# Optimization experiments

Measured on AMD Instinct MI355X. Metric: run time of the kernel, lower is better.

## Reference

```python
import jax, jax.numpy as jnp
import numpy as np

B, L, H, N = 4, 4096, 1024, 64
LN_EPS = 1e-5


def setup_inputs() -> dict:
    key = jax.random.key(0)
    ks = jax.random.split(key, 6)
    x = jax.random.normal(ks[0], (B, L, H), dtype=jnp.float32)
    # S4D-Lin style init
    log_A_real = jnp.log(0.5 * jnp.ones((H, N), dtype=jnp.float32))
    A_imag = jnp.broadcast_to(jnp.pi * jnp.arange(N, dtype=jnp.float32), (H, N))
    C_re = jax.random.normal(ks[1], (H, N), dtype=jnp.float32) * 0.5
    C_im = jax.random.normal(ks[2], (H, N), dtype=jnp.float32) * 0.5
    # dt log-uniform in [1e-3, 1e-1]
    u = jax.random.uniform(ks[3], (H,), dtype=jnp.float32)
    log_dt = u * (jnp.log(0.1) - jnp.log(0.001)) + jnp.log(0.001)
    D = jax.random.normal(ks[4], (H,), dtype=jnp.float32)
    ln_w = jnp.ones((H,), dtype=jnp.float32)
    ln_b = jnp.zeros((H,), dtype=jnp.float32)
    return {"x": x, "log_A_real": log_A_real, "A_imag": A_imag,
            "C_re": C_re, "C_im": C_im, "log_dt": log_dt, "D": D,
            "ln_w": ln_w, "ln_b": ln_b}


def _s4d_kernel(log_A_real, A_imag, C_re, C_im, log_dt, length):
    # A: [H, N] complex with negative real part (stability)
    A = -jnp.exp(log_A_real) + 1j * A_imag
    dt = jnp.exp(log_dt)[:, None]                      # [H, 1]
    dtA = dt * A                                       # [H, N]
    C = C_re + 1j * C_im                               # [H, N]
    # ZOH discretization: Bbar*C -> C * (exp(dtA)-1)/A
    Ct = C * (jnp.exp(dtA) - 1.0) / A                  # [H, N]
    l = jnp.arange(length, dtype=jnp.float32)
    # Vandermonde: exp(dtA * l) over [H, N, L]
    V = jnp.exp(dtA[:, :, None] * l[None, None, :])
    K = 2.0 * jnp.real(jnp.einsum('hn,hnl->hl', Ct, V))  # [H, L]
    return K


def reference(x, log_A_real, A_imag, C_re, C_im, log_dt, D, ln_w, ln_b):
    b, length, h = x.shape
    K = _s4d_kernel(log_A_real, A_imag, C_re, C_im, log_dt, length)  # [H, L]
    # causal convolution via FFT, channels last: x is [B, L, H]
    n = 2 * length
    Xf = jnp.fft.rfft(x, n=n, axis=1)                  # [B, n//2+1, H]
    Kf = jnp.fft.rfft(K, n=n, axis=1)                  # [H, n//2+1]
    y = jnp.fft.irfft(Xf * Kf.T[None, :, :], n=n, axis=1)[:, :length, :]
    z = y + x * D[None, None, :]
    # dropout is identity in eval mode; residual + LayerNorm
    r = x + z
    mu = jnp.mean(r, axis=-1, keepdims=True)
    var = jnp.var(r, axis=-1, keepdims=True)
    out = (r - mu) * jax.lax.rsqrt(var + LN_EPS) * ln_w + ln_b
    return out
```

## Files before the change

kernel.cpp:

```cpp
#include <hip/hip_runtime.h>
#include <cstdint>

#define Bb 4
#define Lseq 4096
#define Hh 1024
#define Nst 64
constexpr float LN_EPS = 1e-5f;

typedef _Float16 f16x8 __attribute__((ext_vector_type(8)));
typedef _Float16 f16x4 __attribute__((ext_vector_type(4)));
typedef float f32x4v __attribute__((ext_vector_type(4)));

__global__ __launch_bounds__(256) void k_precompute(
    const float* __restrict__ logA, const float* __restrict__ Aim,
    const float* __restrict__ Cre, const float* __restrict__ Cim,
    const float* __restrict__ logdt, _Float16* __restrict__ mats,
    float* __restrict__ wwR, float* __restrict__ wwI) {
    __shared__ float sdAr[64], sdAi[64], scR[64], scI[64], sK[64];
    const int h = blockIdx.x, tid = threadIdx.x;
    _Float16* g = mats + (size_t)h * 20480;

    if (tid < 64) {
        const int n = tid, idx = h * 64 + n;
        const float ar = -expf(logA[idx]), ai = Aim[idx];
        const float dt = expf(logdt[h]);
        const float dAr = dt * ar, dAi = dt * ai;
        const float em = expf(dAr);
        const float wr = em * cosf(dAi), wi = em * sinf(dAi);
        const float Er = wr - 1.0f, Ei = wi;
        const float cr = Cre[idx], ci = Cim[idx];
        const float nr = cr * Er - ci * Ei, ni = cr * Ei + ci * Er;
        const float invd = 1.0f / (ar * ar + ai * ai);
        const float CtR = (nr * ar + ni * ai) * invd;
        const float CtI = (ni * ar - nr * ai) * invd;
        sdAr[n] = dAr; sdAi[n] = dAi; scR[n] = 2.0f * CtR; scI[n] = 2.0f * CtI;
        const float e64 = expf(dAr * 64.0f), a64 = dAi * 64.0f;
        wwR[idx] = e64 * cosf(a64);
        wwI[idx] = e64 * sinf(a64);
    }
    __syncthreads();

    for (int e = tid; e < 4096; e += 256) {
        const int row = e >> 6, colj = e & 63;
        {
            const float p = (float)(63 - colj);
            const float ee = expf(sdAr[row] * p), ang = sdAi[row] * p;
            g[e]        = (_Float16)(ee * cosf(ang));
            g[4096 + e] = (_Float16)(ee * sinf(ang));
        }
        {
            const int n = colj;
            const float q = (float)(row + 1);
            const float ee = expf(sdAr[n] * q), ang = sdAi[n] * q;
            const float wRq = ee * cosf(ang), wIq = ee * sinf(ang);
            g[12288 + e] = (_Float16)(scR[n] * wRq - scI[n] * wIq);
            g[16384 + e] = (_Float16)(-(scR[n] * wIq + scI[n] * wRq));
        }
    }
    if (tid < 64) {
        const float tau = (float)tid;
        float sum = 0.0f;
        for (int n = 0; n < 64; ++n) {
            const float ee = expf(sdAr[n] * tau), ang = sdAi[n] * tau;
            sum += ee * (scR[n] * cosf(ang) - scI[n] * sinf(ang));
        }
        sK[tid] = sum;
    }
    __syncthreads();
    for (int e = tid; e < 4096; e += 256) {
        const int t = e >> 6, j = e & 63;
        g[8192 + e] = (j <= t) ? (_Float16)sK[t - j] : (_Float16)0.0f;
    }
}

__global__ __launch_bounds__(256) void k_transpose(const float* __restrict__ x,
                                                   float* __restrict__ xt) {
    __shared__ float tile[32][33];
    const int h0 = blockIdx.x * 32;
    const int l0 = blockIdx.y * 32;
    const int b  = blockIdx.z;
    const int tj = threadIdx.x & 31;
    const int ti = threadIdx.x >> 5;

    const float* src = x + ((size_t)b * Lseq + l0) * Hh + h0;
#pragma unroll
    for (int it = 0; it < 4; ++it) {
        int row = it * 8 + ti;
        tile[row][tj] = src[(size_t)row * Hh + tj];
    }
    __syncthreads();
    float* dst = xt + ((size_t)b * Hh + h0) * Lseq + l0;
#pragma unroll
    for (int it = 0; it < 4; ++it) {
        int row = it * 8 + ti;
        dst[(size_t)row * Lseq + tj] = tile[tj][row];
    }
}

#define XBF   0
#define SRBF  9216
#define SIBF  18432
#define URo   27648
#define UIo   36864
#define uRh   46080
#define uIh   55296
#define M1o   27648
#define PRo   36864
#define PIo   46080
#define YFo   55296

#define AFRAG(base, row0) \
    (*(const f16x8*)(sm + (base) + ((row0) + (lane & 15)) * 144 + kh * 2 + ((lane >> 4) << 4)))

__global__ __launch_bounds__(256, 2) void k_chunk(
    float* __restrict__ xt, const _Float16* __restrict__ mats,
    const float* __restrict__ wwR, const float* __restrict__ wwI,
    const float* __restrict__ Dp) {
    __shared__ __align__(16) unsigned char sm[64512];
    const int tid = threadIdx.x, lane = tid & 63, wv = tid >> 6;
    const int bx = blockIdx.x, h = bx & (Hh - 1), b = bx >> 10;
    float* xr = xt + (size_t)(b * Hh + h) * Lseq;
    const _Float16* g = mats + (size_t)h * 20480;
    const int col = lane & 15, qd = lane >> 4;
    const int band = wv * 16;

#pragma unroll
    for (int r = 0; r < 4; ++r) {
        const int idx = r * 1024 + tid * 4;
        const float4 v = *(const float4*)(xr + idx);
        const int c = idx >> 6, j = idx & 63;
        f16x4 hv;
        hv[0] = (_Float16)v.x; hv[1] = (_Float16)v.y;
        hv[2] = (_Float16)v.z; hv[3] = (_Float16)v.w;
        *(f16x4*)(sm + XBF + c * 144 + j * 2) = hv;
    }
#pragma unroll
    for (int r = 0; r < 4; ++r) {
        const int e = r * 2048 + tid * 8;
        const int m = e >> 12, e2 = e & 4095;
        const int row = e2 >> 6, cc = e2 & 63;
        *(uint4*)(sm + (m ? UIo : URo) + row * 144 + cc * 2) =
            *(const uint4*)(g + e);
    }
    __syncthreads();

    f32x4v aR[4] = {}, aI[4] = {};
#pragma unroll
    for (int kh = 0; kh < 64; kh += 32) {
        const f16x8 ax = AFRAG(XBF, band);
#pragma unroll
        for (int nt = 0; nt < 4; ++nt) {
            aR[nt] = __builtin_amdgcn_mfma_f32_16x16x32_f16(
                ax, AFRAG(URo, nt * 16), aR[nt], 0, 0, 0);
            aI[nt] = __builtin_amdgcn_mfma_f32_16x16x32_f16(
                ax, AFRAG(UIo, nt * 16), aI[nt], 0, 0, 0);
        }
    }
#pragma unroll
    for (int nt = 0; nt < 4; ++nt)
#pragma unroll
        for (int rg = 0; rg < 4; ++rg) {
            const int c = band + qd * 4 + rg, n = nt * 16 + col;
            *(_Float16*)(sm + uRh + c * 144 + n * 2) = (_Float16)aR[nt][rg];
            *(_Float16*)(sm + uIh + c * 144 + n * 2) = (_Float16)aI[nt][rg];
        }
    __syncthreads();

    if (wv < 2) {
        const int n = wv * 32 + (lane & 31);
        const float wR = wwR[h * 64 + n], wI = wwI[h * 64 + n];
        float sR = 0.0f, sI = 0.0f;
        for (int c = 0; c < 64; ++c) {
            if (lane < 32) {
                *(_Float16*)(sm + SRBF + c * 144 + n * 2) = (_Float16)sR;
                *(_Float16*)(sm + SIBF + c * 144 + n * 2) = (_Float16)sI;
            }
            const float uRv = (float)*(const _Float16*)(sm + uRh + c * 144 + n * 2);
            const float uIv = (float)*(const _Float16*)(sm + uIh + c * 144 + n * 2);
            const float nR = fmaf(wR, sR, fmaf(-wI, sI, uRv));
            sI = fmaf(wR, sI, fmaf(wI, sR, uIv));
            sR = nR;
        }
    } else {
        const _Float16* gs = g + (wv == 2 ? 8192 : 12288);
        unsigned char* dst = sm + (wv == 2 ? M1o : PRo);
#pragma unroll
        for (int r = 0; r < 8; ++r) {
            const int e = r * 512 + lane * 8;
            const int row = e >> 6, cc = e & 63;
            *(uint4*)(dst + row * 144 + cc * 2) = *(const uint4*)(gs + e);
        }
    }
    __syncthreads();
#pragma unroll
    for (int r = 0; r < 2; ++r) {
        const int e = r * 2048 + tid * 8;
        const int row = e >> 6, cc = e & 63;
        *(uint4*)(sm + PIo + row * 144 + cc * 2) = *(const uint4*)(g + 16384 + e);
    }
    __syncthreads();

    f32x4v acc[4] = {};
#pragma unroll
    for (int kh = 0; kh < 64; kh += 32) {
        const f16x8 ax = AFRAG(XBF, band);
#pragma unroll
        for (int tt = 0; tt < 4; ++tt)
            acc[tt] = __builtin_amdgcn_mfma_f32_16x16x32_f16(
                ax, AFRAG(M1o, tt * 16), acc[tt], 0, 0, 0);
    }
#pragma unroll
    for (int kh = 0; kh < 64; kh += 32) {
        const f16x8 as = AFRAG(SRBF, band);
#pragma unroll
        for (int tt = 0; tt < 4; ++tt)
            acc[tt] = __builtin_amdgcn_mfma_f32_16x16x32_f16(
                as, AFRAG(PRo, tt * 16), acc[tt], 0, 0, 0);
    }
#pragma unroll
    for (int kh = 0; kh < 64; kh += 32) {
        const f16x8 az = AFRAG(SIBF, band);
#pragma unroll
        for (int tt = 0; tt < 4; ++tt)
            acc[tt] = __builtin_amdgcn_mfma_f32_16x16x32_f16(
                az, AFRAG(PIo, tt * 16), acc[tt], 0, 0, 0);
    }
#pragma unroll
    for (int tt = 0; tt < 4; ++tt)
#pragma unroll
        for (int rg = 0; rg < 4; ++rg) {
            const int c = band + qd * 4 + rg, t = tt * 16 + col;
            *(_Float16*)(sm + YFo + c * 144 + t * 2) = (_Float16)acc[tt][rg];
        }
    __syncthreads();

    const float Dp1 = 1.0f + Dp[h];
#pragma unroll
    for (int r = 0; r < 4; ++r) {
        const int idx = r * 1024 + tid * 4;
        const int c = idx >> 6, j = idx & 63;
        const float4 xv = *(const float4*)(xr + idx);
        const f16x4 yv = *(const f16x4*)(sm + YFo + c * 144 + j * 2);
        float4 o;
        o.x = fmaf(xv.x, Dp1, (float)yv[0]);
        o.y = fmaf(xv.y, Dp1, (float)yv[1]);
        o.z = fmaf(xv.z, Dp1, (float)yv[2]);
        o.w = fmaf(xv.w, Dp1, (float)yv[3]);
        *(float4*)(xr + idx) = o;
    }
}

__global__ __launch_bounds__(256) void k_ln(const float* __restrict__ rt,
                                            float* __restrict__ out,
                                            const float* __restrict__ lnw,
                                            const float* __restrict__ lnb) {
    __shared__ float tile[256 * 33];
    __shared__ float ps[8][32], pq[8][32];
    __shared__ float mm[32], rs[32];
    const int b  = blockIdx.y;
    const int l0 = blockIdx.x * 32;
    const int ll = threadIdx.x & 31;
    const int hh = threadIdx.x >> 5;

    const float* base = rt + (size_t)b * Hh * Lseq + l0;

    float psum = 0.0f, psq = 0.0f;
#pragma unroll 8
    for (int hc = 0; hc < Hh; hc += 8) {
        const float v = base[(size_t)(hc + hh) * Lseq + ll];
        psum += v;
        psq = fmaf(v, v, psq);
    }
    ps[hh][ll] = psum;
    pq[hh][ll] = psq;
    __syncthreads();
    if (threadIdx.x < 32) {
        float s = 0.f, q = 0.f;
#pragma unroll
        for (int k = 0; k < 8; ++k) {
            s += ps[k][threadIdx.x];
            q += pq[k][threadIdx.x];
        }
        const float mu  = s * (1.0f / Hh);
        const float var = fmaf(-mu, mu, q * (1.0f / Hh));
        mm[threadIdx.x] = mu;
        rs[threadIdx.x] = rsqrtf(var + LN_EPS);
    }
    __syncthreads();

    for (int hc = 0; hc < Hh; hc += 256) {
#pragma unroll
        for (int it = 0; it < 32; ++it) {
            const int hrow = it * 8 + hh;
            tile[hrow * 33 + ll] = base[(size_t)(hc + hrow) * Lseq + ll];
        }
        const float w  = lnw[hc + threadIdx.x];
        const float bo = lnb[hc + threadIdx.x];
        __syncthreads();
        float* orow = out + ((size_t)b * Lseq + l0) * Hh + hc + threadIdx.x;
#pragma unroll
        for (int l = 0; l < 32; ++l) {
            const float v = tile[threadIdx.x * 33 + l];
            orow[(size_t)l * Hh] = fmaf((v - mm[l]) * rs[l], w, bo);
        }
        __syncthreads();
    }
}

extern "C" void kernel_launch(void* const* d_in, const int* in_sizes, int n_in,
                              void* d_out, int out_size, void* d_ws, size_t ws_size,
                              hipStream_t stream) {
    const float* x     = (const float*)d_in[0];
    const float* logA  = (const float*)d_in[1];
    const float* Aim   = (const float*)d_in[2];
    const float* Cre   = (const float*)d_in[3];
    const float* Cim   = (const float*)d_in[4];
    const float* logdt = (const float*)d_in[5];
    const float* Dp    = (const float*)d_in[6];
    const float* lnw   = (const float*)d_in[7];
    const float* lnb   = (const float*)d_in[8];
    float* out = (float*)d_out;
    float* ws  = (float*)d_ws;

    _Float16* mats = (_Float16*)d_out;
    float* wwR = (float*)((char*)d_out + 41943040);
    float* wwI = (float*)((char*)d_out + 42205184);

    k_precompute<<<dim3(Hh), 256, 0, stream>>>(logA, Aim, Cre, Cim, logdt,
                                               mats, wwR, wwI);
    k_transpose<<<dim3(Hh / 32, Lseq / 32, Bb), 256, 0, stream>>>(x, ws);
    k_chunk<<<dim3(Bb * Hh), 256, 0, stream>>>(ws, mats, wwR, wwI, Dp);
    k_ln<<<dim3(Lseq / 32, Bb), 256, 0, stream>>>(ws, out, lnw, lnb);
}
```

Baseline: 269.5 us.

## Load MFMA operands directly from global, shrink LDS, and single-pass LayerNorm

The chunk kernel stops staging x and the precomputed matrices in shared memory. It reads MFMA fragments straight from global memory and keeps the x fragments in registers for reuse, which cuts LDS use enough to raise occupancy to four blocks per CU. The LayerNorm kernel now caches each row in LDS during the statistics pass and writes the output from that tile, so the workspace is no longer read twice. The cost is more uncoalesced global fragment loads that rely on the cache, plus a larger LDS tile in the LN kernel.

Result: slower. 293.2 us (+8.8%).

```diff
diff --git a/kernel.cpp b/kernel.cpp
--- a/kernel.cpp
+++ b/kernel.cpp
@@ -97,26 +97,22 @@
     }
 }
 
-#define XBF   0
-#define SRBF  9216
-#define SIBF  18432
-#define URo   27648
-#define UIo   36864
-#define uRh   46080
-#define uIh   55296
-#define M1o   27648
-#define PRo   36864
-#define PIo   46080
-#define YFo   55296
-
-#define AFRAG(base, row0) \
-    (*(const f16x8*)(sm + (base) + ((row0) + (lane & 15)) * 144 + kh * 2 + ((lane >> 4) << 4)))
-
-__global__ __launch_bounds__(256, 2) void k_chunk(
+#define uRo 0
+#define uIo 9216
+#define SRo 18432
+#define SIo 27648
+#define YFo 0
+
+#define GFRAG(p, row0, kk) \
+    (*(const f16x8*)((p) + ((row0) + col) * 64 + (kk) + qd * 8))
+#define LFRAG(base, row0, kk) \
+    (*(const f16x8*)(sm + (base) + ((row0) + col) * 144 + ((kk) + qd * 8) * 2))
+
+__global__ __launch_bounds__(256, 4) void k_chunk(
     float* __restrict__ xt, const _Float16* __restrict__ mats,
     const float* __restrict__ wwR, const float* __restrict__ wwI,
     const float* __restrict__ Dp) {
-    __shared__ __align__(16) unsigned char sm[64512];
+    __shared__ __align__(16) unsigned char sm[36864];
     const int tid = threadIdx.x, lane = tid & 63, wv = tid >> 6;
     const int bx = blockIdx.x, h = bx & (Hh - 1), b = bx >> 10;
     float* xr = xt + (size_t)(b * Hh + h) * Lseq;
@@ -124,36 +120,26 @@
     const int col = lane & 15, qd = lane >> 4;
     const int band = wv * 16;
 
-#pragma unroll
-    for (int r = 0; r < 4; ++r) {
-        const int idx = r * 1024 + tid * 4;
-        const float4 v = *(const float4*)(xr + idx);
-        const int c = idx >> 6, j = idx & 63;
-        f16x4 hv;
-        hv[0] = (_Float16)v.x; hv[1] = (_Float16)v.y;
-        hv[2] = (_Float16)v.z; hv[3] = (_Float16)v.w;
-        *(f16x4*)(sm + XBF + c * 144 + j * 2) = hv;
-    }
-#pragma unroll
-    for (int r = 0; r < 4; ++r) {
-        const int e = r * 2048 + tid * 8;
-        const int m = e >> 12, e2 = e & 4095;
-        const int row = e2 >> 6, cc = e2 & 63;
-        *(uint4*)(sm + (m ? UIo : URo) + row * 144 + cc * 2) =
-            *(const uint4*)(g + e);
-    }
-    __syncthreads();
-
+    f16x8 axk[2];
     f32x4v aR[4] = {}, aI[4] = {};
 #pragma unroll
-    for (int kh = 0; kh < 64; kh += 32) {
-        const f16x8 ax = AFRAG(XBF, band);
+    for (int kh2 = 0; kh2 < 2; ++kh2) {
+        const int kk = kh2 * 32;
+        const float* xp = xr + (band + col) * 64 + kk + qd * 8;
+        const float4 v0 = *(const float4*)(xp);
+        const float4 v1 = *(const float4*)(xp + 4);
+        f16x8 a;
+        a[0] = (_Float16)v0.x; a[1] = (_Float16)v0.y;
+        a[2] = (_Float16)v0.z; a[3] = (_Float16)v0.w;
+        a[4] = (_Float16)v1.x; a[5] = (_Float16)v1.y;
+        a[6] = (_Float16)v1.z; a[7] = (_Float16)v1.w;
+        axk[kh2] = a;
 #pragma unroll
         for (int nt = 0; nt < 4; ++nt) {
             aR[nt] = __builtin_amdgcn_mfma_f32_16x16x32_f16(
-                ax, AFRAG(URo, nt * 16), aR[nt], 0, 0, 0);
+                a, GFRAG(g, nt * 16, kk), aR[nt], 0, 0, 0);
             aI[nt] = __builtin_amdgcn_mfma_f32_16x16x32_f16(
-                ax, AFRAG(UIo, nt * 16), aI[nt], 0, 0, 0);
+                a, GFRAG(g + 4096, nt * 16, kk), aI[nt], 0, 0, 0);
         }
     }
 #pragma unroll
@@ -161,8 +147,8 @@
 #pragma unroll
         for (int rg = 0; rg < 4; ++rg) {
             const int c = band + qd * 4 + rg, n = nt * 16 + col;
-            *(_Float16*)(sm + uRh + c * 144 + n * 2) = (_Float16)aR[nt][rg];
-            *(_Float16*)(sm + uIh + c * 144 + n * 2) = (_Float16)aI[nt][rg];
+            *(_Float16*)(sm + uRo + c * 144 + n * 2) = (_Float16)aR[nt][rg];
+            *(_Float16*)(sm + uIo + c * 144 + n * 2) = (_Float16)aI[nt][rg];
         }
     __syncthreads();
 
@@ -172,59 +158,46 @@
         float sR = 0.0f, sI = 0.0f;
         for (int c = 0; c < 64; ++c) {
             if (lane < 32) {
-                *(_Float16*)(sm + SRBF + c * 144 + n * 2) = (_Float16)sR;
-                *(_Float16*)(sm + SIBF + c * 144 + n * 2) = (_Float16)sI;
+                *(_Float16*)(sm + SRo + c * 144 + n * 2) = (_Float16)sR;
+                *(_Float16*)(sm + SIo + c * 144 + n * 2) = (_Float16)sI;
             }
-            const float uRv = (float)*(const _Float16*)(sm + uRh + c * 144 + n * 2);
-            const float uIv = (float)*(const _Float16*)(sm + uIh + c * 144 + n * 2);
+            const float uRv = (float)*(const _Float16*)(sm + uRo + c * 144 + n * 2);
+            const float uIv = (float)*(const _Float16*)(sm + uIo + c * 144 + n * 2);
             const float nR = fmaf(wR, sR, fmaf(-wI, sI, uRv));
             sI = fmaf(wR, sI, fmaf(wI, sR, uIv));
             sR = nR;
         }
-    } else {
-        const _Float16* gs = g + (wv == 2 ? 8192 : 12288);
-        unsigned char* dst = sm + (wv == 2 ? M1o : PRo);
-#pragma unroll
-        for (int r = 0; r < 8; ++r) {
-            const int e = r * 512 + lane * 8;
-            const int row = e >> 6, cc = e & 63;
-            *(uint4*)(dst + row * 144 + cc * 2) = *(const uint4*)(gs + e);
-        }
-    }
-    __syncthreads();
-#pragma unroll
-    for (int r = 0; r < 2; ++r) {
-        const int e = r * 2048 + tid * 8;
-        const int row = e >> 6, cc = e & 63;
-        *(uint4*)(sm + PIo + row * 144 + cc * 2) = *(const uint4*)(g + 16384 + e);
     }
     __syncthreads();
 
     f32x4v acc[4] = {};
 #pragma unroll
-    for (int kh = 0; kh < 64; kh += 32) {
-        const f16x8 ax = AFRAG(XBF, band);
+    for (int kh2 = 0; kh2 < 2; ++kh2) {
+        const int kk = kh2 * 32;
 #pragma unroll
         for (int tt = 0; tt < 4; ++tt)
             acc[tt] = __builtin_amdgcn_mfma_f32_16x16x32_f16(
-                ax, AFRAG(M1o, tt * 16), acc[tt], 0, 0, 0);
-    }
-#pragma unroll
-    for (int kh = 0; kh < 64; kh += 32) {
-        const f16x8 as = AFRAG(SRBF, band);
+                axk[kh2], GFRAG(g + 8192, tt * 16, kk), acc[tt], 0, 0, 0);
+    }
+#pragma unroll
+    for (int kh2 = 0; kh2 < 2; ++kh2) {
+        const int kk = kh2 * 32;
+        const f16x8 as = LFRAG(SRo, band, kk);
 #pragma unroll
         for (int tt = 0; tt < 4; ++tt)
             acc[tt] = __builtin_amdgcn_mfma_f32_16x16x32_f16(
-                as, AFRAG(PRo, tt * 16), acc[tt], 0, 0, 0);
-    }
-#pragma unroll
-    for (int kh = 0; kh < 64; kh += 32) {
-        const f16x8 az = AFRAG(SIBF, band);
+                as, GFRAG(g + 12288, tt * 16, kk), acc[tt], 0, 0, 0);
+    }
+#pragma unroll
+    for (int kh2 = 0; kh2 < 2; ++kh2) {
+        const int kk = kh2 * 32;
+        const f16x8 az = LFRAG(SIo, band, kk);
 #pragma unroll
         for (int tt = 0; tt < 4; ++tt)
             acc[tt] = __builtin_amdgcn_mfma_f32_16x16x32_f16(
-                az, AFRAG(PIo, tt * 16), acc[tt], 0, 0, 0);
-    }
+                az, GFRAG(g + 16384, tt * 16, kk), acc[tt], 0, 0, 0);
+    }
+    __syncthreads();
 #pragma unroll
     for (int tt = 0; tt < 4; ++tt)
 #pragma unroll
@@ -250,60 +223,56 @@
     }
 }
 
-__global__ __launch_bounds__(256) void k_ln(const float* __restrict__ rt,
-                                            float* __restrict__ out,
-                                            const float* __restrict__ lnw,
-                                            const float* __restrict__ lnb) {
-    __shared__ float tile[256 * 33];
-    __shared__ float ps[8][32], pq[8][32];
-    __shared__ float mm[32], rs[32];
+__global__ __launch_bounds__(512, 2) void k_ln(const float* __restrict__ rt,
+                                               float* __restrict__ out,
+                                               const float* __restrict__ lnw,
+                                               const float* __restrict__ lnb) {
+    __shared__ float tile[16 * 1032];
+    __shared__ float ps[32][17], pq[32][17];
+    __shared__ float mm[16], rs[16];
     const int b  = blockIdx.y;
-    const int l0 = blockIdx.x * 32;
-    const int ll = threadIdx.x & 31;
-    const int hh = threadIdx.x >> 5;
+    const int l0 = blockIdx.x * 16;
+    const int tid = threadIdx.x;
+    const int ll = tid & 15;
+    const int hh = tid >> 4;
 
     const float* base = rt + (size_t)b * Hh * Lseq + l0;
 
     float psum = 0.0f, psq = 0.0f;
 #pragma unroll 8
-    for (int hc = 0; hc < Hh; hc += 8) {
+    for (int hc = 0; hc < Hh; hc += 32) {
         const float v = base[(size_t)(hc + hh) * Lseq + ll];
+        tile[ll * 1032 + hc + hh] = v;
         psum += v;
         psq = fmaf(v, v, psq);
     }
     ps[hh][ll] = psum;
     pq[hh][ll] = psq;
     __syncthreads();
-    if (threadIdx.x < 32) {
+    if (tid < 16) {
         float s = 0.f, q = 0.f;
 #pragma unroll
-        for (int k = 0; k < 8; ++k) {
-            s += ps[k][threadIdx.x];
-            q += pq[k][threadIdx.x];
+        for (int k = 0; k < 32; ++k) {
+            s += ps[k][tid];
+            q += pq[k][tid];
         }
         const float mu  = s * (1.0f / Hh);
         const float var = fmaf(-mu, mu, q * (1.0f / Hh));
-        mm[threadIdx.x] = mu;
-        rs[threadIdx.x] = rsqrtf(var + LN_EPS);
-    }
-    __syncthreads();
-
-    for (int hc = 0; hc < Hh; hc += 256) {
-#pragma unroll
-        for (int it = 0; it < 32; ++it) {
-            const int hrow = it * 8 + hh;
-            tile[hrow * 33 + ll] = base[(size_t)(hc + hrow) * Lseq + ll];
-        }
-        const float w  = lnw[hc + threadIdx.x];
-        const float bo = lnb[hc + threadIdx.x];
-        __syncthreads();
-        float* orow = out + ((size_t)b * Lseq + l0) * Hh + hc + threadIdx.x;
-#pragma unroll
-        for (int l = 0; l < 32; ++l) {
-            const float v = tile[threadIdx.x * 33 + l];
-            orow[(size_t)l * Hh] = fmaf((v - mm[l]) * rs[l], w, bo);
-        }
-        __syncthreads();
+        mm[tid] = mu;
+        rs[tid] = rsqrtf(var + LN_EPS);
+    }
+    __syncthreads();
+
+    const float w0 = lnw[tid],       b0 = lnb[tid];
+    const float w1 = lnw[512 + tid], b1 = lnb[512 + tid];
+    float* obase = out + ((size_t)b * Lseq + l0) * Hh;
+#pragma unroll 4
+    for (int l = 0; l < 16; ++l) {
+        const float mu = mm[l], rsg = rs[l];
+        const float v0 = tile[l * 1032 + tid];
+        const float v1 = tile[l * 1032 + 512 + tid];
+        obase[(size_t)l * Hh + tid]       = fmaf((v0 - mu) * rsg, w0, b0);
+        obase[(size_t)l * Hh + 512 + tid] = fmaf((v1 - mu) * rsg, w1, b1);
     }
 }
 
@@ -330,5 +299,5 @@
                                                mats, wwR, wwI);
     k_transpose<<<dim3(Hh / 32, Lseq / 32, Bb), 256, 0, stream>>>(x, ws);
     k_chunk<<<dim3(Bb * Hh), 256, 0, stream>>>(ws, mats, wwR, wwI, Dp);
-    k_ln<<<dim3(Lseq / 32, Bb), 256, 0, stream>>>(ws, out, lnw, lnb);
-}
+    k_ln<<<dim3(Lseq / 16, Bb), 512, 0, stream>>>(ws, out, lnw, lnb);
+}
```
